# Kernel tuning notes

Measured on AMD Instinct MI355X. Metric: run time of the kernel, lower is better.

Reference implementation:

```python
import jax, jax.numpy as jnp
import numpy as np

EMB = 1024
FF = 4 * EMB

def _ternary(w):
    # BitNet b1.58 absmean quantization; forward uses pure ternary weights
    scale = jnp.maximum(jnp.mean(jnp.abs(w)), 1e-8)
    w_t = jnp.clip(jnp.round(w / scale), -1.0, 1.0)
    # STE: forward = w_t, backward = identity w.r.t. w
    return w + jax.lax.stop_gradient(w_t - w)

def setup_inputs() -> dict:
    key = jax.random.key(0)
    kx, k1, k2, kb1, kb2 = jax.random.split(key, 5)
    x = jax.random.normal(kx, (4, 2048, EMB), dtype=jnp.float32)
    # nn.Linear default init: U(-1/sqrt(fan_in), 1/sqrt(fan_in))
    lim1 = 1.0 / np.sqrt(EMB)
    lim2 = 1.0 / np.sqrt(FF)
    W1 = jax.random.uniform(k1, (FF, EMB), jnp.float32, -lim1, lim1)
    b1 = jax.random.uniform(kb1, (FF,), jnp.float32, -lim1, lim1)
    W2 = jax.random.uniform(k2, (EMB, FF), jnp.float32, -lim2, lim2)
    b2 = jax.random.uniform(kb2, (EMB,), jnp.float32, -lim2, lim2)
    return {"x": x, "W1": W1, "b1": b1, "W2": W2, "b2": b2}

def reference(x, W1, b1, W2, b2):
    h = jnp.einsum('bsd,fd->bsf', x, _ternary(W1)) + b1  # [B,S,FF]
    h = jax.nn.gelu(h, approximate=False)  # torch nn.GELU default = exact erf
    out = jnp.einsum('bsf,df->bsd', h, _ternary(W2)) + b2  # [B,S,EMB]
    return out
```

## Files before the change

### kernel.cpp

```cpp
#include <hip/hip_runtime.h>
#include <hip/hip_bf16.h>
#include <cstdint>
#include <cstddef>

typedef __bf16 bf16x8 __attribute__((ext_vector_type(8)));
typedef float  f32x4  __attribute__((ext_vector_type(4)));

__device__ __forceinline__ unsigned short f2bf(float f) {
    __hip_bfloat16 b = __float2bfloat16(f);
    return *reinterpret_cast<unsigned short*>(&b);
}


__global__ void zero2_kernel(float* p) {
    if (threadIdx.x < 2) p[threadIdx.x] = 0.0f;
}

__global__ void abs_sum2_kernel(const float4* __restrict__ w0, const float4* __restrict__ w1,
                                int n4, float* __restrict__ out) {
    int half = (int)blockIdx.x >> 9;
    const float4* w = half ? w1 : w0;
    int b = (int)blockIdx.x & 511;
    float s = 0.0f;
    for (int i = b * blockDim.x + threadIdx.x; i < n4; i += 512 * blockDim.x) {
        float4 v = w[i];
        s += fabsf(v.x) + fabsf(v.y) + fabsf(v.z) + fabsf(v.w);
    }
    #pragma unroll
    for (int o = 32; o > 0; o >>= 1) s += __shfl_down(s, o, 64);
    __shared__ float part[4];
    int lane = threadIdx.x & 63, wid = threadIdx.x >> 6;
    if (lane == 0) part[wid] = s;
    __syncthreads();
    if (threadIdx.x == 0) atomicAdd(&out[half], part[0] + part[1] + part[2] + part[3]);
}

__global__ void ternarize2_kernel(const float4* __restrict__ w0, ushort4* __restrict__ t0,
                                  const float4* __restrict__ w1, ushort4* __restrict__ t1,
                                  int n4, const float* __restrict__ sum, float inv_n) {
    int half = (int)blockIdx.x >> 10;
    const float4* w = half ? w1 : w0;
    ushort4* t = half ? t1 : t0;
    int b = (int)blockIdx.x & 1023;
    float scale = fmaxf(sum[half] * inv_n, 1e-8f);
    float inv = 1.0f / scale;
    for (int i = b * blockDim.x + threadIdx.x; i < n4; i += 1024 * blockDim.x) {
        float4 v = w[i];
        ushort4 o;
        o.x = f2bf(fminf(fmaxf(rintf(v.x * inv), -1.0f), 1.0f));
        o.y = f2bf(fminf(fmaxf(rintf(v.y * inv), -1.0f), 1.0f));
        o.z = f2bf(fminf(fmaxf(rintf(v.z * inv), -1.0f), 1.0f));
        o.w = f2bf(fminf(fmaxf(rintf(v.w * inv), -1.0f), 1.0f));
        t[i] = o;
    }
}

__global__ void cvt_bf16_kernel(const float4* __restrict__ in, ushort4* __restrict__ out, int n4) {
    for (int i = blockIdx.x * blockDim.x + threadIdx.x; i < n4; i += gridDim.x * blockDim.x) {
        float4 v = in[i];
        ushort4 o;
        o.x = f2bf(v.x); o.y = f2bf(v.y); o.z = f2bf(v.z); o.w = f2bf(v.w);
        out[i] = o;
    }
}


template <int EPI>
__global__ __launch_bounds__(256)
void gemm_bt_kernel(const unsigned short* __restrict__ A,
                    const unsigned short* __restrict__ B,
                    const float* __restrict__ bias,
                    void* __restrict__ C,
                    int K, int N) {
    __shared__ __align__(16) unsigned short As[128 * 64];
    __shared__ __align__(16) unsigned short Bs[128 * 64];

    const int tid  = threadIdx.x;
    const int lane = tid & 63;
    const int wid  = tid >> 6;
    const int wr   = wid >> 1;
    const int wc   = wid & 1;
    const int mBase = wr * 64;
    const int nBase = wc * 64;
    const int lr = lane & 15;
    const int lq = lane >> 4;

    const size_t aRow0 = (size_t)blockIdx.y * 128;
    const size_t bRow0 = (size_t)blockIdx.x * 128;

    f32x4 acc[4][4];
    #pragma unroll
    for (int i = 0; i < 4; ++i)
        #pragma unroll
        for (int j = 0; j < 4; ++j)
            acc[i][j] = f32x4{0.f, 0.f, 0.f, 0.f};

    for (int k0 = 0; k0 < K; k0 += 64) {
        __syncthreads();
        #pragma unroll
        for (int t = 0; t < 4; ++t) {
            int chunk = t * 256 + tid;
            int r = chunk >> 3;
            int cc = chunk & 7;
            int c = ((cc ^ (r & 7)) << 3);
            const unsigned short* ga = A + (aRow0 + r) * (size_t)K + k0 + c;
            const unsigned short* gb = B + (bRow0 + r) * (size_t)K + k0 + c;
            __builtin_amdgcn_global_load_lds(
                (__attribute__((address_space(1))) void*)ga,
                (__attribute__((address_space(3))) void*)(&As[chunk * 8]), 16, 0, 0);
            __builtin_amdgcn_global_load_lds(
                (__attribute__((address_space(1))) void*)gb,
                (__attribute__((address_space(3))) void*)(&Bs[chunk * 8]), 16, 0, 0);
        }
        __syncthreads();
        #pragma unroll
        for (int ks = 0; ks < 2; ++ks) {
            const int swz = (((ks * 4 + lq) ^ (lr & 7)) << 3);
            bf16x8 avec[4], bvec[4];
            #pragma unroll
            for (int i = 0; i < 4; ++i) {
                avec[i] = *(const bf16x8*)&As[(mBase + i * 16 + lr) * 64 + swz];
                bvec[i] = *(const bf16x8*)&Bs[(nBase + i * 16 + lr) * 64 + swz];
            }
            #pragma unroll
            for (int mi = 0; mi < 4; ++mi)
                #pragma unroll
                for (int ni = 0; ni < 4; ++ni)
                    acc[mi][ni] = __builtin_amdgcn_mfma_f32_16x16x32_bf16(
                        avec[mi], bvec[ni], acc[mi][ni], 0, 0, 0);
        }
    }

    #pragma unroll
    for (int mi = 0; mi < 4; ++mi) {
        #pragma unroll
        for (int ni = 0; ni < 4; ++ni) {
            int col = (int)bRow0 + nBase + ni * 16 + lr;
            float bv = bias[col];
            #pragma unroll
            for (int r = 0; r < 4; ++r) {
                size_t row = aRow0 + mBase + mi * 16 + lq * 4 + r;
                float v = acc[mi][ni][r] + bv;
                if (EPI == 0) {
                    v = 0.5f * v * (1.0f + erff(v * 0.70710678118f));
                    ((unsigned short*)C)[row * (size_t)N + col] = f2bf(v);
                } else {
                    ((float*)C)[row * (size_t)N + col] = v;
                }
            }
        }
    }
}


extern "C" void kernel_launch(void* const* d_in, const int* in_sizes, int n_in,
                              void* d_out, int out_size, void* d_ws, size_t ws_size,
                              hipStream_t stream) {
    const float* x  = (const float*)d_in[0];
    const float* W1 = (const float*)d_in[1];
    const float* b1 = (const float*)d_in[2];
    const float* W2 = (const float*)d_in[3];
    const float* b2 = (const float*)d_in[4];
    float* out = (float*)d_out;

    const int M = 8192, EMB = 1024, FF = 4096;
    const int nW = FF * EMB;

    char* ws = (char*)d_ws;
    float* sums = (float*)ws;
    unsigned short* W1t = (unsigned short*)(ws + 256);
    unsigned short* W2t = W1t + (size_t)nW;
    unsigned short* xb  = W2t + (size_t)nW;
    unsigned short* h   = xb  + (size_t)M * EMB;

    zero2_kernel<<<1, 64, 0, stream>>>(sums);
    abs_sum2_kernel<<<1024, 256, 0, stream>>>((const float4*)W1, (const float4*)W2,
                                              nW / 4, sums);
    ternarize2_kernel<<<2048, 256, 0, stream>>>((const float4*)W1, (ushort4*)W1t,
                                                (const float4*)W2, (ushort4*)W2t,
                                                nW / 4, sums, 1.0f / nW);
    cvt_bf16_kernel<<<2048, 256, 0, stream>>>((const float4*)x, (ushort4*)xb,
                                              (M * EMB) / 4);

    gemm_bt_kernel<0><<<dim3(FF / 128, M / 128), 256, 0, stream>>>(xb, W1t, b1, h, EMB, FF);
    gemm_bt_kernel<1><<<dim3(EMB / 128, M / 128), 256, 0, stream>>>(h, W2t, b2, out, FF, EMB);
}
```

Baseline: 299.9 us.

## Fuse prep kernels, templatize GEMM dims, and use fast exp-based GELU

Merges weight ternarization and activation bf16 conversion into a single launch. Makes GEMM K and N compile-time constants, hoists global/LDS address computation out of the k-loop and unrolls it by two. Replaces the exact erf GELU with an exp2/rcp sigmoid-form approximation to cut epilogue cost, which adds small numerical deviation from exact GELU.

Result: faster. 279.9 us (-6.7%).

```diff
diff --git a/kernel.cpp b/kernel.cpp
--- a/kernel.cpp
+++ b/kernel.cpp
@@ -9,6 +9,13 @@
 __device__ __forceinline__ unsigned short f2bf(float f) {
     __hip_bfloat16 b = __float2bfloat16(f);
     return *reinterpret_cast<unsigned short*>(&b);
+}
+
+__device__ __forceinline__ float fast_gelu(float x) {
+    float x2 = x * x;
+    float m  = x * __builtin_fmaf(x2, -0.10294314f, -2.30220795f);
+    float e  = __builtin_amdgcn_exp2f(m);
+    return x * __builtin_amdgcn_rcpf(1.0f + e);
 }
 
 
@@ -35,16 +42,28 @@
     if (threadIdx.x == 0) atomicAdd(&out[half], part[0] + part[1] + part[2] + part[3]);
 }
 
-__global__ void ternarize2_kernel(const float4* __restrict__ w0, ushort4* __restrict__ t0,
-                                  const float4* __restrict__ w1, ushort4* __restrict__ t1,
-                                  int n4, const float* __restrict__ sum, float inv_n) {
-    int half = (int)blockIdx.x >> 10;
-    const float4* w = half ? w1 : w0;
-    ushort4* t = half ? t1 : t0;
+__global__ void prep_kernel(const float4* __restrict__ w0, ushort4* __restrict__ t0,
+                            const float4* __restrict__ w1, ushort4* __restrict__ t1,
+                            int n4w,
+                            const float4* __restrict__ x, ushort4* __restrict__ xb,
+                            int n4x,
+                            const float* __restrict__ sum, float inv_n) {
+    int seg = (int)blockIdx.x >> 10;
     int b = (int)blockIdx.x & 1023;
-    float scale = fmaxf(sum[half] * inv_n, 1e-8f);
+    if (seg == 2) {
+        for (int i = b * blockDim.x + threadIdx.x; i < n4x; i += 1024 * blockDim.x) {
+            float4 v = x[i];
+            ushort4 o;
+            o.x = f2bf(v.x); o.y = f2bf(v.y); o.z = f2bf(v.z); o.w = f2bf(v.w);
+            xb[i] = o;
+        }
+        return;
+    }
+    const float4* w = seg ? w1 : w0;
+    ushort4* t = seg ? t1 : t0;
+    float scale = fmaxf(sum[seg] * inv_n, 1e-8f);
     float inv = 1.0f / scale;
-    for (int i = b * blockDim.x + threadIdx.x; i < n4; i += 1024 * blockDim.x) {
+    for (int i = b * blockDim.x + threadIdx.x; i < n4w; i += 1024 * blockDim.x) {
         float4 v = w[i];
         ushort4 o;
         o.x = f2bf(fminf(fmaxf(rintf(v.x * inv), -1.0f), 1.0f));
@@ -55,23 +74,13 @@
     }
 }
 
-__global__ void cvt_bf16_kernel(const float4* __restrict__ in, ushort4* __restrict__ out, int n4) {
-    for (int i = blockIdx.x * blockDim.x + threadIdx.x; i < n4; i += gridDim.x * blockDim.x) {
-        float4 v = in[i];
-        ushort4 o;
-        o.x = f2bf(v.x); o.y = f2bf(v.y); o.z = f2bf(v.z); o.w = f2bf(v.w);
-        out[i] = o;
-    }
-}
-
-
-template <int EPI>
+
+template <int EPI, int K, int N>
 __global__ __launch_bounds__(256)
 void gemm_bt_kernel(const unsigned short* __restrict__ A,
                     const unsigned short* __restrict__ B,
                     const float* __restrict__ bias,
-                    void* __restrict__ C,
-                    int K, int N) {
+                    void* __restrict__ C) {
     __shared__ __align__(16) unsigned short As[128 * 64];
     __shared__ __align__(16) unsigned short Bs[128 * 64];
 
@@ -88,6 +97,13 @@
     const size_t aRow0 = (size_t)blockIdx.y * 128;
     const size_t bRow0 = (size_t)blockIdx.x * 128;
 
+    const int rA  = tid >> 3;
+    const int cSw = (((tid & 7) ^ (rA & 7)) << 3);
+    const unsigned short* ga = A + (aRow0 + rA) * (size_t)K + cSw;
+    const unsigned short* gb = B + (bRow0 + rA) * (size_t)K + cSw;
+    unsigned short* ldsA = &As[tid * 8];
+    unsigned short* ldsB = &Bs[tid * 8];
+
     f32x4 acc[4][4];
     #pragma unroll
     for (int i = 0; i < 4; ++i)
@@ -95,27 +111,27 @@
         for (int j = 0; j < 4; ++j)
             acc[i][j] = f32x4{0.f, 0.f, 0.f, 0.f};
 
+    const int swz0 = ((lq ^ (lr & 7)) << 3);
+    const int swz1 = (((4 + lq) ^ (lr & 7)) << 3);
+
+    #pragma unroll 2
     for (int k0 = 0; k0 < K; k0 += 64) {
         __syncthreads();
         #pragma unroll
         for (int t = 0; t < 4; ++t) {
-            int chunk = t * 256 + tid;
-            int r = chunk >> 3;
-            int cc = chunk & 7;
-            int c = ((cc ^ (r & 7)) << 3);
-            const unsigned short* ga = A + (aRow0 + r) * (size_t)K + k0 + c;
-            const unsigned short* gb = B + (bRow0 + r) * (size_t)K + k0 + c;
             __builtin_amdgcn_global_load_lds(
-                (__attribute__((address_space(1))) void*)ga,
-                (__attribute__((address_space(3))) void*)(&As[chunk * 8]), 16, 0, 0);
+                (const __attribute__((address_space(1))) void*)(ga + (size_t)t * 32 * K),
+                (__attribute__((address_space(3))) void*)(ldsA + t * 2048), 16, 0, 0);
             __builtin_amdgcn_global_load_lds(
-                (__attribute__((address_space(1))) void*)gb,
-                (__attribute__((address_space(3))) void*)(&Bs[chunk * 8]), 16, 0, 0);
-        }
+                (const __attribute__((address_space(1))) void*)(gb + (size_t)t * 32 * K),
+                (__attribute__((address_space(3))) void*)(ldsB + t * 2048), 16, 0, 0);
+        }
+        ga += 64;
+        gb += 64;
         __syncthreads();
         #pragma unroll
         for (int ks = 0; ks < 2; ++ks) {
-            const int swz = (((ks * 4 + lq) ^ (lr & 7)) << 3);
+            const int swz = ks ? swz1 : swz0;
             bf16x8 avec[4], bvec[4];
             #pragma unroll
             for (int i = 0; i < 4; ++i) {
@@ -142,8 +158,7 @@
                 size_t row = aRow0 + mBase + mi * 16 + lq * 4 + r;
                 float v = acc[mi][ni][r] + bv;
                 if (EPI == 0) {
-                    v = 0.5f * v * (1.0f + erff(v * 0.70710678118f));
-                    ((unsigned short*)C)[row * (size_t)N + col] = f2bf(v);
+                    ((unsigned short*)C)[row * (size_t)N + col] = f2bf(fast_gelu(v));
                 } else {
                     ((float*)C)[row * (size_t)N + col] = v;
                 }
@@ -176,12 +191,11 @@
     zero2_kernel<<<1, 64, 0, stream>>>(sums);
     abs_sum2_kernel<<<1024, 256, 0, stream>>>((const float4*)W1, (const float4*)W2,
                                               nW / 4, sums);
-    ternarize2_kernel<<<2048, 256, 0, stream>>>((const float4*)W1, (ushort4*)W1t,
-                                                (const float4*)W2, (ushort4*)W2t,
-                                                nW / 4, sums, 1.0f / nW);
-    cvt_bf16_kernel<<<2048, 256, 0, stream>>>((const float4*)x, (ushort4*)xb,
-                                              (M * EMB) / 4);
-
-    gemm_bt_kernel<0><<<dim3(FF / 128, M / 128), 256, 0, stream>>>(xb, W1t, b1, h, EMB, FF);
-    gemm_bt_kernel<1><<<dim3(EMB / 128, M / 128), 256, 0, stream>>>(h, W2t, b2, out, FF, EMB);
-}
+    prep_kernel<<<3072, 256, 0, stream>>>((const float4*)W1, (ushort4*)W1t,
+                                          (const float4*)W2, (ushort4*)W2t, nW / 4,
+                                          (const float4*)x, (ushort4*)xb, (M * EMB) / 4,
+                                          sums, 1.0f / nW);
+
+    gemm_bt_kernel<0, 1024, 4096><<<dim3(FF / 128, M / 128), 256, 0, stream>>>(xb, W1t, b1, h);
+    gemm_bt_kernel<1, 4096, 1024><<<dim3(EMB / 128, M / 128), 256, 0, stream>>>(h, W2t, b2, out);
+}
```
